# Kernel tuning notes

Hardware: AMD Instinct MI355X
Metric: run time of the kernel (lower is better)

The kernel has to match this reference:

```python
import jax, jax.numpy as jnp
import numpy as np

# Fixed hyperparameters from init_kwargs
KH, KW = 3, 3
GRID_SIZE = 5
SPLINE_ORDER = 3
GRID_RANGE = (-1.0, 1.0)


def _make_grid():
    # grid buffer: arange(-k, grid_size + k + 1) * h + grid_range[0], shape (G + 2k + 1,) = (12,)
    h = (GRID_RANGE[1] - GRID_RANGE[0]) / GRID_SIZE
    return (jnp.arange(-SPLINE_ORDER, GRID_SIZE + SPLINE_ORDER + 1, dtype=jnp.float32) * h
            + GRID_RANGE[0])


def _unfold(x):
    # torch.nn.Unfold with kernel (3,3), stride 1, pad 0, dilation 1.
    # Returns (N, C*KH*KW) with channel-major ordering (c, i, j), matching torch.
    B, C, H, W = x.shape
    Ho, Wo = H - KH + 1, W - KW + 1
    cols = [x[:, :, i:i + Ho, j:j + Wo] for i in range(KH) for j in range(KW)]
    p = jnp.stack(cols, axis=2)                    # (B, C, KH*KW, Ho, Wo)
    p = p.reshape(B, C * KH * KW, Ho * Wo)         # (B, in_features, L)
    p = p.transpose(0, 2, 1).reshape(-1, C * KH * KW)  # (B*L, in_features)
    return p, Ho, Wo


def _b_splines(x, grid):
    # x: (N, in_features); grid: (G + 2k + 1,) uniform, shared across features.
    # Returns (N, in_features, G + k) B-spline basis via Cox-de Boor recursion.
    x = x[..., None]  # (N, in, 1)
    bases = ((x >= grid[:-1]) & (x < grid[1:])).astype(x.dtype)  # (N, in, G+2k)
    for k in range(1, SPLINE_ORDER + 1):
        left = (x - grid[: -(k + 1)]) / (grid[k:-1] - grid[: -(k + 1)])
        right = (grid[k + 1:] - x) / (grid[k + 1:] - grid[1:-k])
        bases = left * bases[..., :-1] + right * bases[..., 1:]
    return bases  # (N, in, G + k)


def setup_inputs() -> dict:
    key = jax.random.key(0)
    k1, k2, k3, k4 = jax.random.split(key, 4)
    in_features = 32 * KH * KW  # 288
    out_features = 64
    n_coef = GRID_SIZE + SPLINE_ORDER  # 8
    x = jax.random.normal(k1, (16, 32, 64, 64), dtype=jnp.float32)
    base_weight = jax.random.normal(k2, (out_features, in_features), dtype=jnp.float32) * (1.0 / np.sqrt(in_features))
    spline_weight = jax.random.normal(k3, (out_features, in_features, n_coef), dtype=jnp.float32) * 0.1
    spline_scaler = jax.random.normal(k4, (out_features, in_features), dtype=jnp.float32) * (1.0 / np.sqrt(in_features))
    return {"x": x, "base_weight": base_weight, "spline_weight": spline_weight,
            "spline_scaler": spline_scaler}


def reference(x, base_weight, spline_weight, spline_scaler):
    B = x.shape[0]
    out_features = base_weight.shape[0]
    grid = _make_grid()

    patches, Ho, Wo = _unfold(x)                              # (N, in_features)
    N, in_features = patches.shape

    # KANLinear forward
    base_out = jnp.matmul(jax.nn.relu(patches), base_weight.T)  # (N, out)
    bases = _b_splines(patches, grid)                           # (N, in, G+k)
    scaled_w = spline_weight * spline_scaler[..., None]         # (out, in, G+k)
    spline_out = jnp.matmul(bases.reshape(N, -1), scaled_w.reshape(out_features, -1).T)
    out = base_out + spline_out                                 # (N, out)

    out = out.reshape(B, Ho, Wo, out_features).transpose(0, 3, 1, 2)  # (B, C_out, Ho, Wo)
    return out
```

## Files before the change

kernel.cpp:

```cpp
#include <hip/hip_runtime.h>
#include <stdint.h>

typedef _Float16 half8  __attribute__((ext_vector_type(8)));
typedef float    f32x4  __attribute__((ext_vector_type(4)));
typedef uint32_t u32x4  __attribute__((ext_vector_type(4)));

#define FIN  288
#define NOUT 64
#define LPB  3844
#define KSPL 72
#define NBF  20736
#define NBAS (16*64*32*64)

#define SC   200
#define LDSN 6432

#define LDSL (31*SC + 2*64 + 64 + 8)


__device__ inline half8 bspline8(float xv) {
  float u = fmaf(xv, 2.5f, 5.5f);
  float fi = floorf(u);
  int i = (int)fi;
  float t = u - fi, s = 1.0f - t;
  float t2 = t * t, t3 = t2 * t;
  float s2 = s * s, s3 = s2 * s;
  float w3 = t3 * 0.16666667f;
  float w0 = s3 * 0.16666667f;
  float w1 = fmaf(0.5f, t3, -t2) + 0.66666667f;
  float w2 = fmaf(0.5f, s3, -s2) + 0.66666667f;
  uint32_t u01 = __builtin_bit_cast(uint32_t, __builtin_amdgcn_cvt_pkrtz(w0, w1));
  uint32_t u23 = __builtin_bit_cast(uint32_t, __builtin_amdgcn_cvt_pkrtz(w2, w3));
  uint64_t V = (uint64_t)u01 | ((uint64_t)u23 << 32);
  uint32_t vl = (uint32_t)(V << 16);
  u32x4 fr;
#pragma unroll
  for (int q = 0; q < 4; ++q) {
    int d = i - 2 * q;
    uint32_t rr = (uint32_t)(V >> ((48 - 16 * d) & 63));
    fr[q] = ((uint32_t)d <= 3u) ? rr : ((d == 4) ? vl : 0u);
  }
  return __builtin_bit_cast(half8, fr);
}

__global__ __launch_bounds__(256) void prep_all(const float* __restrict__ x,
                                                const float* __restrict__ bw,
                                                const float* __restrict__ sw,
                                                const float* __restrict__ sc,
                                                half8* __restrict__ ws) {
  int bid = blockIdx.x;
  if (bid < 2048) {
    int t = bid * 256 + threadIdx.x;
    int w4 = t & 15;
    int cperm = (t >> 4) & 31;
    int bh = t >> 9;
    int c = ((cperm & 7) << 2) | (cperm >> 3);
    const float4 v = *(const float4*)(x + (bh >> 6) * 131072 + c * 4096 +
                                      (bh & 63) * 64 + w4 * 4);
    half8* dst = ws + NBF + (size_t)t * 4;
    dst[0] = bspline8(v.x);
    dst[1] = bspline8(v.y);
    dst[2] = bspline8(v.z);
    dst[3] = bspline8(v.w);
  } else {
    int t = (bid - 2048) * 256 + threadIdx.x;
    half8 v;
    int dst;
    if (t < NOUT * FIN) {
      int o = t / FIN;
      int f = t - o * FIN;
      float scale = sc[t];
      const float* p = sw + t * 8;
#pragma unroll
      for (int c = 0; c < 8; ++c) v[c] = (_Float16)(p[c] * scale);
      int ch = f / 9;
      int r  = f - ch * 9;
      int ii = r / 3;
      int jj = r - ii * 3;
      int g  = ch >> 2, q = ch & 3;
      int kt = ii * 24 + jj * 8 + g;
      dst = (kt * 4 + (o >> 4)) * 64 + q * 16 + (o & 15);
    } else {
      int t2 = t - NOUT * FIN;
      int lane = t2 & 63;
      int nf = (t2 >> 6) & 3;
      int ktb = t2 >> 8;
      int o = nf * 16 + (lane & 15);
      int q = lane >> 4;
      int i2 = ktb / 3;
      int j2 = ktb - 3 * i2;
#pragma unroll
      for (int c0 = 0; c0 < 8; ++c0)
        v[c0] = (_Float16)bw[o * FIN + 9 * (q * 8 + c0) + 3 * i2 + j2];
      dst = ((KSPL + ktb) * 4 + nf) * 64 + lane;
    }
    ws[dst] = v;
  }
}

__global__ __launch_bounds__(256, 4) void kan_main(
    const float* __restrict__ x,
    const half8* __restrict__ ws,
    float* __restrict__ out) {
  __shared__ float lx[LDSN];
  const half8* __restrict__ bfrag = ws;
  const half8* __restrict__ bas   = ws + NBF;

  const int tid = threadIdx.x;
  int bid0 = blockIdx.x;
  int bid = (bid0 & 7) * 124 + (bid0 >> 3);
  const int b  = bid / 62;
  const int ho = bid - b * 62;

  const float* xb = x + b * 131072 + ho * 64;
#pragma unroll
  for (int r = 0; r < 6; ++r) {
    int gid = r * 256 + tid;
    int row = gid >> 4;
    int c   = (row * 683) >> 11;
    int ii  = row - c * 3;
    int colv = (gid & 15) * 4;
    const float4 v = *(const float4*)(xb + c * 4096 + ii * 64 + colv);
    *(float4*)(&lx[c * SC + (c >> 3) * 8 + ii * 64 + colv]) = v;
  }

  const int lane = tid & 63;
  const int wv   = tid >> 6;
  const int quad = lane >> 4;
  const int m16  = lane & 15;
  const int wo   = wv * 16 + m16;

  f32x4 acc[4];
#pragma unroll
  for (int nf = 0; nf < 4; ++nf) acc[nf] = (f32x4){0.f, 0.f, 0.f, 0.f};

  const half8* bb = bas + (size_t)((b * 64 + ho) * 32 + quad * 8) * 64 + wo;
  int kt = 0;
#pragma unroll
  for (int ii = 0; ii < 3; ++ii) {
#pragma unroll
    for (int jj = 0; jj < 3; ++jj) {
      const half8* p = bb + ii * 2048 + jj;
#pragma unroll
      for (int g = 0; g < 8; ++g) {
        half8 af = p[g * 64];
#pragma unroll
        for (int nf = 0; nf < 4; ++nf) {
          half8 bf = bfrag[(kt * 4 + nf) * 64 + lane];
          acc[nf] = __builtin_amdgcn_mfma_f32_16x16x32_f16(af, bf, acc[nf], 0, 0, 0);
        }
        ++kt;
      }
    }
  }

  __syncthreads();

  const float* lb = lx + quad * (8 * SC) + quad * 8 + wo;
#pragma unroll
  for (int kb = 0; kb < 9; ++kb) {
    const int i2 = kb / 3;
    const int j2 = kb - 3 * i2;
    half8 a;
#pragma unroll
    for (int j = 0; j < 8; ++j)
      a[j] = (_Float16)fmaxf(lb[j * SC + i2 * 64 + j2], 0.0f);
#pragma unroll
    for (int nf = 0; nf < 4; ++nf) {
      half8 bf = bfrag[((KSPL + kb) * 4 + nf) * 64 + lane];
      acc[nf] = __builtin_amdgcn_mfma_f32_16x16x32_f16(a, bf, acc[nf], 0, 0, 0);
    }
  }

  float* ob = out + b * (NOUT * LPB) + ho * 62;
#pragma unroll
  for (int rg = 0; rg < 4; ++rg) {
    int wo2 = wv * 16 + quad * 4 + rg;
    if (wo2 < 62) {
#pragma unroll
      for (int nf = 0; nf < 4; ++nf) {
        int o = nf * 16 + m16;
        ob[o * LPB + wo2] = acc[nf][rg];
      }
    }
  }
}

__global__ void prep_bfrag_legacy(const float* __restrict__ bw,
                                  const float* __restrict__ sw,
                                  const float* __restrict__ sc,
                                  half8* __restrict__ bfrag) {
  int t = blockIdx.x * 256 + threadIdx.x;
  half8 v;
  int dst;
  if (t < NOUT * FIN) {
    int o = t / FIN;
    int f = t - o * FIN;
    float scale = sc[t];
    const float* p = sw + t * 8;
#pragma unroll
    for (int c = 0; c < 8; ++c) v[c] = (_Float16)(p[c] * scale);
    int ch = f / 9;
    int r  = f - ch * 9;
    int ii = r / 3;
    int jj = r - ii * 3;
    int g  = ch >> 2, q = ch & 3;
    int kt = ii * 24 + jj * 8 + g;
    dst = (kt * 4 + (o >> 4)) * 64 + q * 16 + (o & 15);
  } else {
    int t2 = t - NOUT * FIN;
    int lane = t2 & 63;
    int nf = (t2 >> 6) & 3;
    int ktb = t2 >> 8;
    int o = nf * 16 + (lane & 15);
    int f0 = ktb * 32 + (lane >> 4) * 8;
    const float* p = bw + o * FIN + f0;
#pragma unroll
    for (int c = 0; c < 8; ++c) v[c] = (_Float16)p[c];
    dst = ((KSPL + ktb) * 4 + nf) * 64 + lane;
  }
  bfrag[dst] = v;
}

__global__ __launch_bounds__(256, 4) void kan_main_legacy(
    const float* __restrict__ x,
    const half8* __restrict__ bfrag,
    float* __restrict__ out) {
  __shared__ float lx[LDSL];
  const int tid = threadIdx.x;
  const int bid = blockIdx.x;
  const int b  = bid / 62;
  const int ho = bid - b * 62;
  const float* xb = x + b * 131072 + ho * 64;
#pragma unroll
  for (int r = 0; r < 6; ++r) {
    int gid = r * 256 + tid;
    int row = gid >> 4;
    int c   = (row * 683) >> 11;
    int ii  = row - c * 3;
    int colv = (gid & 15) * 4;
    const float4 v = *(const float4*)(xb + c * 4096 + ii * 64 + colv);
    *(float4*)(&lx[c * SC + ii * 64 + colv]) = v;
  }
  __syncthreads();
  const int lane = tid & 63;
  const int wv   = tid >> 6;
  const int quad = lane >> 4;
  const int m16  = lane & 15;
  const int wo   = wv * 16 + m16;
  f32x4 acc[4];
#pragma unroll
  for (int nf = 0; nf < 4; ++nf) acc[nf] = (f32x4){0.f, 0.f, 0.f, 0.f};
  int kt = 0;
#pragma unroll
  for (int ii = 0; ii < 3; ++ii) {
#pragma unroll
    for (int jj = 0; jj < 3; ++jj) {
      const float* lbase = lx + quad * SC + ii * 64 + wo + jj;
#pragma unroll
      for (int g = 0; g < 8; ++g) {
        float xv = lbase[g * (4 * SC)];
        half8 af = bspline8(xv);
#pragma unroll
        for (int nf = 0; nf < 4; ++nf) {
          half8 bf = bfrag[(kt * 4 + nf) * 64 + lane];
          acc[nf] = __builtin_amdgcn_mfma_f32_16x16x32_f16(af, bf, acc[nf], 0, 0, 0);
        }
        ++kt;
      }
    }
  }
#pragma unroll
  for (int kb = 0; kb < 9; ++kb) {
    int f0 = kb * 32 + quad * 8;
    half8 a;
#pragma unroll
    for (int j = 0; j < 8; ++j) {
      int f = f0 + j;
      int c = (f * 57) >> 9;
      int r = f - c * 9;
      int i2 = (r * 11) >> 5;
      int j2 = r - i2 * 3;
      a[j] = (_Float16)fmaxf(lx[c * SC + i2 * 64 + wo + j2], 0.0f);
    }
#pragma unroll
    for (int nf = 0; nf < 4; ++nf) {
      half8 bf = bfrag[((KSPL + kb) * 4 + nf) * 64 + lane];
      acc[nf] = __builtin_amdgcn_mfma_f32_16x16x32_f16(a, bf, acc[nf], 0, 0, 0);
    }
  }
  float* ob = out + b * (NOUT * LPB) + ho * 62;
#pragma unroll
  for (int rg = 0; rg < 4; ++rg) {
    int wo2 = wv * 16 + quad * 4 + rg;
    if (wo2 < 62) {
#pragma unroll
      for (int nf = 0; nf < 4; ++nf) {
        int o = nf * 16 + m16;
        ob[o * LPB + wo2] = acc[nf][rg];
      }
    }
  }
}

extern "C" void kernel_launch(void* const* d_in, const int* in_sizes, int n_in,
                              void* d_out, int out_size, void* d_ws, size_t ws_size,
                              hipStream_t stream) {
  const float* x  = (const float*)d_in[0];
  const float* bw = (const float*)d_in[1];
  const float* sw = (const float*)d_in[2];
  const float* sc = (const float*)d_in[3];
  float* out = (float*)d_out;
  half8* ws = (half8*)d_ws;

  const size_t need = (size_t)(NBF + NBAS) * sizeof(half8);
  if (ws_size >= need) {
    prep_all<<<2048 + 81, 256, 0, stream>>>(x, bw, sw, sc, ws);
    kan_main<<<16 * 62, 256, 0, stream>>>(x, ws, out);
  } else {
    prep_bfrag_legacy<<<81, 256, 0, stream>>>(bw, sw, sc, ws);
    kan_main_legacy<<<16 * 62, 256, 0, stream>>>(x, ws, out);
  }
}
```

Baseline: 142.3 us.

## Precompute relu fp16 activations in prep and tile 4 M-tiles per wave

The prep kernel gains a third phase that writes ReLU'd fp16 packed x fragments to workspace, so the main kernel no longer stages x through LDS or needs a block barrier. The main kernel now gives each wave a full output row (4 M-tiles of 16 columns) with a 4x4 accumulator array, reusing each weight fragment load across four MFMAs. The grid shrinks to 256 blocks with occupancy hint 1. This trades more workspace traffic and fewer resident waves for fewer weight reloads, and the clamped last row does redundant work.

```diff
diff --git a/kernel.cpp b/kernel.cpp
--- a/kernel.cpp
+++ b/kernel.cpp
@@ -11,11 +11,11 @@
 #define KSPL 72
 #define NBF  20736
 #define NBAS (16*64*32*64)
-
-#define SC   200
-#define LDSN 6432
-
-#define LDSL (31*SC + 2*64 + 64 + 8)
+#define NXR  (16*64*64*4)
+#define PADS 16
+
+#define SCL  200
+#define LDSL (31*SCL + 2*64 + 64 + 8)
 
 
 __device__ inline half8 bspline8(float xv) {
@@ -62,8 +62,18 @@
     dst[1] = bspline8(v.y);
     dst[2] = bspline8(v.z);
     dst[3] = bspline8(v.w);
+  } else if (bid < 3072) {
+    int t = (bid - 2048) * 256 + threadIdx.x;
+    int quad = t & 3;
+    int w = (t >> 2) & 63;
+    int bh = t >> 8;
+    const float* xp = x + (bh >> 6) * 131072 + (quad * 8) * 4096 + (bh & 63) * 64 + w;
+    half8 v;
+#pragma unroll
+    for (int j = 0; j < 8; ++j) v[j] = (_Float16)fmaxf(xp[j * 4096], 0.0f);
+    ws[NBF + NBAS + t] = v;
   } else {
-    int t = (bid - 2048) * 256 + threadIdx.x;
+    int t = (bid - 3072) * 256 + threadIdx.x;
     half8 v;
     int dst;
     if (t < NOUT * FIN) {
@@ -98,89 +108,84 @@
   }
 }
 
-__global__ __launch_bounds__(256, 4) void kan_main(
-    const float* __restrict__ x,
+__global__ __launch_bounds__(256, 1) void kan_main(
     const half8* __restrict__ ws,
     float* __restrict__ out) {
-  __shared__ float lx[LDSN];
   const half8* __restrict__ bfrag = ws;
   const half8* __restrict__ bas   = ws + NBF;
+  const half8* __restrict__ xr    = ws + NBF + NBAS;
 
   const int tid = threadIdx.x;
   int bid0 = blockIdx.x;
-  int bid = (bid0 & 7) * 124 + (bid0 >> 3);
-  const int b  = bid / 62;
-  const int ho = bid - b * 62;
-
-  const float* xb = x + b * 131072 + ho * 64;
-#pragma unroll
-  for (int r = 0; r < 6; ++r) {
-    int gid = r * 256 + tid;
-    int row = gid >> 4;
-    int c   = (row * 683) >> 11;
-    int ii  = row - c * 3;
-    int colv = (gid & 15) * 4;
-    const float4 v = *(const float4*)(xb + c * 4096 + ii * 64 + colv);
-    *(float4*)(&lx[c * SC + (c >> 3) * 8 + ii * 64 + colv]) = v;
-  }
+  int bid = (bid0 & 7) * 32 + (bid0 >> 3);
+  const int b  = bid >> 4;
+  const int hg = bid & 15;
 
   const int lane = tid & 63;
   const int wv   = tid >> 6;
   const int quad = lane >> 4;
   const int m16  = lane & 15;
-  const int wo   = wv * 16 + m16;
-
-  f32x4 acc[4];
-#pragma unroll
-  for (int nf = 0; nf < 4; ++nf) acc[nf] = (f32x4){0.f, 0.f, 0.f, 0.f};
-
-  const half8* bb = bas + (size_t)((b * 64 + ho) * 32 + quad * 8) * 64 + wo;
-  int kt = 0;
-#pragma unroll
+  const int ho   = hg * 4 + wv;
+  const int hoc  = ho < 61 ? ho : 61;
+
+  f32x4 acc[4][4];
+#pragma unroll
+  for (int mt = 0; mt < 4; ++mt)
+#pragma unroll
+    for (int nf = 0; nf < 4; ++nf) acc[mt][nf] = (f32x4){0.f, 0.f, 0.f, 0.f};
+
+  const half8* bb = bas + ((b * 64 + hoc) * 32 + quad * 8) * 64 + m16;
   for (int ii = 0; ii < 3; ++ii) {
-#pragma unroll
     for (int jj = 0; jj < 3; ++jj) {
-      const half8* p = bb + ii * 2048 + jj;
+      const half8* p   = bb + ii * 2048 + jj;
+      const half8* bfp = bfrag + (ii * 24 + jj * 8) * 256 + lane;
 #pragma unroll
       for (int g = 0; g < 8; ++g) {
-        half8 af = p[g * 64];
+        half8 af[4];
+#pragma unroll
+        for (int mt = 0; mt < 4; ++mt) af[mt] = p[g * 64 + mt * 16];
 #pragma unroll
         for (int nf = 0; nf < 4; ++nf) {
-          half8 bf = bfrag[(kt * 4 + nf) * 64 + lane];
-          acc[nf] = __builtin_amdgcn_mfma_f32_16x16x32_f16(af, bf, acc[nf], 0, 0, 0);
+          half8 bf = bfp[g * 256 + nf * 64];
+#pragma unroll
+          for (int mt = 0; mt < 4; ++mt)
+            acc[mt][nf] = __builtin_amdgcn_mfma_f32_16x16x32_f16(af[mt], bf, acc[mt][nf], 0, 0, 0);
         }
-        ++kt;
       }
     }
   }
 
-  __syncthreads();
-
-  const float* lb = lx + quad * (8 * SC) + quad * 8 + wo;
-#pragma unroll
   for (int kb = 0; kb < 9; ++kb) {
-    const int i2 = kb / 3;
-    const int j2 = kb - 3 * i2;
-    half8 a;
-#pragma unroll
-    for (int j = 0; j < 8; ++j)
-      a[j] = (_Float16)fmaxf(lb[j * SC + i2 * 64 + j2], 0.0f);
+    int i2 = (kb * 11) >> 5;
+    int j2 = kb - 3 * i2;
+    const half8* q = xr + ((b * 64 + hoc + i2) * 64 + m16 + j2) * 4 + quad;
+    half8 af[4];
+#pragma unroll
+    for (int mt = 0; mt < 4; ++mt) af[mt] = q[mt * 64];
+    const half8* bfp = bfrag + (KSPL + kb) * 256 + lane;
 #pragma unroll
     for (int nf = 0; nf < 4; ++nf) {
-      half8 bf = bfrag[((KSPL + kb) * 4 + nf) * 64 + lane];
-      acc[nf] = __builtin_amdgcn_mfma_f32_16x16x32_f16(a, bf, acc[nf], 0, 0, 0);
-    }
-  }
-
-  float* ob = out + b * (NOUT * LPB) + ho * 62;
-#pragma unroll
-  for (int rg = 0; rg < 4; ++rg) {
-    int wo2 = wv * 16 + quad * 4 + rg;
-    if (wo2 < 62) {
-#pragma unroll
-      for (int nf = 0; nf < 4; ++nf) {
-        int o = nf * 16 + m16;
-        ob[o * LPB + wo2] = acc[nf][rg];
+      half8 bf = bfp[nf * 64];
+#pragma unroll
+      for (int mt = 0; mt < 4; ++mt)
+        acc[mt][nf] = __builtin_amdgcn_mfma_f32_16x16x32_f16(af[mt], bf, acc[mt][nf], 0, 0, 0);
+    }
+  }
+
+  if (ho < 62) {
+    float* ob = out + b * (NOUT * LPB) + ho * 62;
+#pragma unroll
+    for (int mt = 0; mt < 4; ++mt) {
+#pragma unroll
+      for (int rg = 0; rg < 4; ++rg) {
+        int wo2 = mt * 16 + quad * 4 + rg;
+        if (wo2 < 62) {
+#pragma unroll
+          for (int nf = 0; nf < 4; ++nf) {
+            int o = nf * 16 + m16;
+            ob[o * LPB + wo2] = acc[mt][nf][rg];
+          }
+        }
       }
     }
   }
@@ -240,7 +245,7 @@
     int ii  = row - c * 3;
     int colv = (gid & 15) * 4;
     const float4 v = *(const float4*)(xb + c * 4096 + ii * 64 + colv);
-    *(float4*)(&lx[c * SC + ii * 64 + colv]) = v;
+    *(float4*)(&lx[c * SCL + ii * 64 + colv]) = v;
   }
   __syncthreads();
   const int lane = tid & 63;
@@ -256,10 +261,10 @@
   for (int ii = 0; ii < 3; ++ii) {
 #pragma unroll
     for (int jj = 0; jj < 3; ++jj) {
-      const float* lbase = lx + quad * SC + ii * 64 + wo + jj;
+      const float* lbase = lx + quad * SCL + ii * 64 + wo + jj;
 #pragma unroll
       for (int g = 0; g < 8; ++g) {
-        float xv = lbase[g * (4 * SC)];
+        float xv = lbase[g * (4 * SCL)];
         half8 af = bspline8(xv);
 #pragma unroll
         for (int nf = 0; nf < 4; ++nf) {
@@ -281,7 +286,7 @@
       int r = f - c * 9;
       int i2 = (r * 11) >> 5;
       int j2 = r - i2 * 3;
-      a[j] = (_Float16)fmaxf(lx[c * SC + i2 * 64 + wo + j2], 0.0f);
+      a[j] = (_Float16)fmaxf(lx[c * SCL + i2 * 64 + wo + j2], 0.0f);
     }
 #pragma unroll
     for (int nf = 0; nf < 4; ++nf) {
@@ -313,10 +318,10 @@
   float* out = (float*)d_out;
   half8* ws = (half8*)d_ws;
 
-  const size_t need = (size_t)(NBF + NBAS) * sizeof(half8);
+  const size_t need = (size_t)(NBF + NBAS + NXR + PADS) * sizeof(half8);
   if (ws_size >= need) {
-    prep_all<<<2048 + 81, 256, 0, stream>>>(x, bw, sw, sc, ws);
-    kan_main<<<16 * 62, 256, 0, stream>>>(x, ws, out);
+    prep_all<<<3153, 256, 0, stream>>>(x, bw, sw, sc, ws);
+    kan_main<<<256, 256, 0, stream>>>(ws, out);
   } else {
     prep_bfrag_legacy<<<81, 256, 0, stream>>>(bw, sw, sc, ws);
     kan_main_legacy<<<16 * 62, 256, 0, stream>>>(x, ws, out);
```

Result: slower. 180.7 us (+27.0%).
